# Optimization experiments

Measured on AMD Instinct MI355X. Metric: run time of the kernel, lower is better.

The kernel has to match this reference:

```python
import jax, jax.numpy as jnp
import numpy as np

K = 3.0  # power parameter k from __init__

def _weight1_sq(d2, r):
    # weight1 on squared distances: (1 - (d/r)^2)^k where d < r, else 0
    r2 = r * r
    flag = d2 < r2
    base = jnp.where(flag, 1.0 - d2 / r2, 0.0)  # >= 0 where flag
    return jnp.where(flag, base ** K, 0.0)

def _weight2(d, r):
    half = r * 0.5
    in1 = d < half
    in2 = (d >= half) & (d < r)
    d_safe = jnp.where(in2, d, half)  # keep base in [0,1] outside the branch
    t = (2.0 * d_safe - r) / r
    w2 = (1.0 - t * t) ** K
    return jnp.where(in1, 1.0, jnp.where(in2, w2, 0.0))

def _normalize(w):
    return w / jnp.sum(w, axis=0, keepdims=True)


def setup_inputs() -> dict:
    key = jax.random.key(0)
    n, p = 4096, 64
    x = jax.random.normal(key, (n, p), dtype=jnp.float32)
    return {
        "x": x,
        "r0": jnp.float32(12.0),
        "r1": jnp.float32(11.0),
        "r2": jnp.float32(12.0),
    }


def reference(x, r0, r1, r2):
    y = x  # y = x.clone(); purely functional here
    sq = jnp.sum(x * x, axis=1)
    # squared pairwise distances (cdist^2), clamped for numerical safety
    d2 = jnp.maximum(sq[:, None] + sq[None, :] - 2.0 * (x @ x.T), 0.0)  # (n, n)
    max_dist = jnp.sqrt(jnp.max(d2))
    # parameter reassignment r := min(r, max_dist)
    r0 = jnp.minimum(r0, max_dist)
    r1 = jnp.minimum(r1, max_dist)
    r2 = jnp.minimum(r2, max_dist)
    # row selection inds: dist[i,i] = 0 <= r0 always, so all rows are kept (identity)
    alpha = _normalize(_weight1_sq(d2, r0))  # (n, n)
    mu = alpha.T @ x  # (n, p)
    mu = jnp.where(jnp.isnan(mu), y, mu)
    U = y - mu  # (n, p), contraction directions
    # projection[i,j] = c_ij * U_j with c_ij = (x_i - y_j) . U_j
    c = x @ U.T - jnp.sum(y * U, axis=1)[None, :]  # (n, n)
    du = c * c * jnp.sum(U * U, axis=1)[None, :]   # ||projection||^2, (n, n)
    du = jnp.maximum(du, 1e-6)
    dv = jnp.sqrt(jnp.maximum(d2 - du, 1e-6))
    du = jnp.sqrt(du)
    beta = _normalize(_weight2(dv, r1) * _weight2(du, r2))  # (n, n)
    e_Z = beta.T @ x  # (n, p)
    return jnp.where(jnp.isnan(e_Z), y, e_Z)
```

## Files before the change

kernel.cpp:

```cpp
#include <hip/hip_runtime.h>
#include <stdint.h>

typedef unsigned short u16;
typedef short bf16x8 __attribute__((ext_vector_type(8)));
typedef unsigned short u16x4 __attribute__((ext_vector_type(4)));
typedef float f32x4 __attribute__((ext_vector_type(4)));

#define NROW 4096
#define LDW 72
#define SLICE 262144
#define NSPLIT 8

__device__ __forceinline__ u16 f2bf(float f) {
  uint32_t u = __float_as_uint(f);
  u = (u + 0x7fffu + ((u >> 16) & 1u)) >> 16;
  return (u16)u;
}

__device__ __forceinline__ u16 f2bf_t(float f) {
  return (u16)(__float_as_uint(f) >> 16);
}

__device__ __forceinline__ f32x4 mfma16(bf16x8 a, bf16x8 b, f32x4 c) {
  return __builtin_amdgcn_mfma_f32_16x16x32_bf16(a, b, c, 0, 0, 0);
}

__device__ __forceinline__ bf16x8 ld8(const u16* p) {
  return *reinterpret_cast<const bf16x8*>(p);
}

__device__ __forceinline__ float fast_sqrt(float x) {
  return __builtin_amdgcn_sqrtf(x);
}

__device__ __forceinline__ float slots_max(const float* __restrict__ maxslots, int lane) {
  float md = maxslots[lane * 16];
#pragma unroll
  for (int o = 1; o < 64; o <<= 1) md = fmaxf(md, __shfl_xor(md, o));
  return md;
}

__global__ __launch_bounds__(256) void prep_kernel(const float* __restrict__ x,
                                                   u16* __restrict__ xb, u16* __restrict__ xT,
                                                   float* __restrict__ sq,
                                                   float* __restrict__ maxslots) {
  __shared__ u16 lt[64 * 68];
  __shared__ float pmax[4];
  const int tid = threadIdx.x, w = tid >> 6, lane = tid & 63;
  const int r0 = blockIdx.x * 64;
  const int rl = tid >> 2;
  const int g = tid & 3;
  const int row = r0 + rl;

  const float* xr = x + row * 64 + g * 16;
  const float* x0 = x + g * 16;
  float s = 0.f, s2 = 0.f;
  u16 bb[16];
#pragma unroll
  for (int k = 0; k < 4; ++k) {
    float4 v = *reinterpret_cast<const float4*>(xr + k * 4);
    float4 z = *reinterpret_cast<const float4*>(x0 + k * 4);
    s += v.x * v.x + v.y * v.y + v.z * v.z + v.w * v.w;
    float dx = v.x - z.x, dy = v.y - z.y, dz = v.z - z.z, dw = v.w - z.w;
    s2 += dx * dx + dy * dy + dz * dz + dw * dw;
    bb[k * 4 + 0] = f2bf(v.x);
    bb[k * 4 + 1] = f2bf(v.y);
    bb[k * 4 + 2] = f2bf(v.z);
    bb[k * 4 + 3] = f2bf(v.w);
  }
#pragma unroll
  for (int k = 0; k < 4; ++k) {
    u16x4 p;
    p[0] = bb[k * 4]; p[1] = bb[k * 4 + 1]; p[2] = bb[k * 4 + 2]; p[3] = bb[k * 4 + 3];
    *reinterpret_cast<u16x4*>(&xb[row * 64 + g * 16 + k * 4]) = p;
  }
#pragma unroll
  for (int k = 0; k < 16; ++k) lt[(g * 16 + k) * 68 + rl] = bb[k];
  s += __shfl_xor(s, 1);
  s += __shfl_xor(s, 2);
  s2 += __shfl_xor(s2, 1);
  s2 += __shfl_xor(s2, 2);
  if (g == 0) sq[row] = s;
  float wm = s2;
#pragma unroll
  for (int o = 4; o < 64; o <<= 1) wm = fmaxf(wm, __shfl_xor(wm, o));
  if (lane == 0) pmax[w] = wm;
  __syncthreads();
#pragma unroll
  for (int cc = 0; cc < 16; ++cc) {
    int c = w * 16 + cc;
    xT[c * NROW + r0 + lane] = lt[c * 68 + lane];
  }
  if (tid == 0)
    maxslots[blockIdx.x * 16] = fmaxf(fmaxf(pmax[0], pmax[1]), fmaxf(pmax[2], pmax[3]));
}

__global__ __launch_bounds__(256) void pass1_max(const u16* __restrict__ xb,
                                                 const float* __restrict__ sq,
                                                 float* __restrict__ maxslots,
                                                 const float* __restrict__ r0in,
                                                 const float* __restrict__ r1in,
                                                 const float* __restrict__ r2in) {
  __shared__ float red[4];
  int w = threadIdx.x >> 6, lane = threadIdx.x & 63;
  {
    float lb = slots_max(maxslots, lane);
    float rmax = fmaxf(fmaxf(r0in[0], r1in[0]), r2in[0]);
    if (lb >= rmax * rmax) return;
  }
  int l16 = lane & 15, quad = lane >> 4;
  int ti = blockIdx.x;
  int i0 = ti * 64 + w * 16;
  bf16x8 a0 = ld8(xb + (i0 + l16) * 64 + quad * 8);
  bf16x8 a1 = ld8(xb + (i0 + l16) * 64 + 32 + quad * 8);
  float sqi[4];
#pragma unroll
  for (int r = 0; r < 4; ++r) sqi[r] = sq[i0 + quad * 4 + r];
  float m = 0.f;
  const int jbase = blockIdx.y * 256;
#pragma unroll
  for (int jb = 0; jb < 4; ++jb) {
    int j0 = jbase + jb * 64;
#pragma unroll
    for (int jt = 0; jt < 4; ++jt) {
      int jr = j0 + jt * 16 + l16;
      bf16x8 b0 = ld8(xb + jr * 64 + quad * 8);
      bf16x8 b1 = ld8(xb + jr * 64 + 32 + quad * 8);
      f32x4 g = {0.f, 0.f, 0.f, 0.f};
      g = mfma16(a0, b0, g);
      g = mfma16(a1, b1, g);
      float sj = sq[jr];
#pragma unroll
      for (int r = 0; r < 4; ++r) m = fmaxf(m, fmaf(-2.f, g[r], sqi[r] + sj));
    }
  }
  m = fmaxf(m, 0.f);
#pragma unroll
  for (int o = 1; o < 64; o <<= 1) m = fmaxf(m, __shfl_xor(m, o));
  if (lane == 0) red[w] = m;
  __syncthreads();
  if (threadIdx.x == 0) {
    m = fmaxf(fmaxf(red[0], red[1]), fmaxf(red[2], red[3]));
    atomicMax((int*)&maxslots[ti * 16], __float_as_int(m));
  }
}

__global__ __launch_bounds__(256, 2) void pass2_kernel(
    const u16* __restrict__ xb, const u16* __restrict__ xT, const float* __restrict__ sq,
    const float* __restrict__ maxslots, const float* __restrict__ r0in,
    float* __restrict__ mu_part, float* __restrict__ s_part) {
  __shared__ u16 ldsw[2][64 * LDW];
  __shared__ u16 xjt[64 * LDW];
  __shared__ float sred[4][64];
  const int tid = threadIdx.x, w = tid >> 6, lane = tid & 63;
  const int l16 = lane & 15, quad = lane >> 4;
  const int j0 = blockIdx.x * 64;
  const int ibase = blockIdx.y * 512;

#pragma unroll
  for (int k = 0; k < 2; ++k) {
    int ch = tid + k * 256;
    int row = ch >> 3, c8 = ch & 7;
    *reinterpret_cast<bf16x8*>(&xjt[row * LDW + c8 * 8]) = ld8(xb + (j0 + row) * 64 + c8 * 8);
  }

  const float md = slots_max(maxslots, lane);
  const float r0c = fminf(r0in[0], fast_sqrt(md));
  const float invr0sq = 1.f / (r0c * r0c);

  float sqj[4];
#pragma unroll
  for (int jt = 0; jt < 4; ++jt) sqj[jt] = sq[j0 + jt * 16 + l16];

  f32x4 zero4 = {0.f, 0.f, 0.f, 0.f};
  f32x4 acc[4];
#pragma unroll
  for (int pt = 0; pt < 4; ++pt) acc[pt] = zero4;
  float sa[4] = {0.f, 0.f, 0.f, 0.f};

  auto do_weights = [&](bf16x8 A0, bf16x8 A1, float4 QI, u16* wbuf) {
#pragma unroll
    for (int jp = 0; jp < 2; ++jp) {
      const int jt0 = jp * 2, jt1 = jp * 2 + 1;
      f32x4 g0 = zero4, g1 = zero4;
      bf16x8 x00 = ld8(&xjt[(jt0 * 16 + l16) * LDW + quad * 8]);
      bf16x8 x10 = ld8(&xjt[(jt1 * 16 + l16) * LDW + quad * 8]);
      bf16x8 x01 = ld8(&xjt[(jt0 * 16 + l16) * LDW + 32 + quad * 8]);
      bf16x8 x11 = ld8(&xjt[(jt1 * 16 + l16) * LDW + 32 + quad * 8]);
      g0 = mfma16(A0, x00, g0);
      g1 = mfma16(A0, x10, g1);
      g0 = mfma16(A1, x01, g0);
      g1 = mfma16(A1, x11, g1);
      u16x4 pk0, pk1;
#pragma unroll
      for (int r = 0; r < 4; ++r) {
        float d2a = fmaxf(fmaf(-2.f, g0[r], QI[r] + sqj[jt0]), 0.f);
        float ba = fmaxf(fmaf(-d2a, invr0sq, 1.f), 0.f);
        float wa = ba * ba * ba;
        sa[jt0] += wa;
        pk0[r] = f2bf_t(wa);
        float d2b = fmaxf(fmaf(-2.f, g1[r], QI[r] + sqj[jt1]), 0.f);
        float bb = fmaxf(fmaf(-d2b, invr0sq, 1.f), 0.f);
        float wb = bb * bb * bb;
        sa[jt1] += wb;
        pk1[r] = f2bf_t(wb);
      }
      *reinterpret_cast<u16x4*>(&wbuf[(jt0 * 16 + l16) * LDW + w * 16 + quad * 4]) = pk0;
      *reinterpret_cast<u16x4*>(&wbuf[(jt1 * 16 + l16) * LDW + w * 16 + quad * 4]) = pk1;
    }
  };

  const int ir0 = ibase + w * 16;
  bf16x8 p0 = ld8(xb + (ir0 + l16) * 64 + quad * 8);
  bf16x8 p1 = ld8(xb + (ir0 + l16) * 64 + 32 + quad * 8);
  float4 q0 = *reinterpret_cast<const float4*>(&sq[ir0 + quad * 4]);
  __syncthreads();
  do_weights(p0, p1, q0, &ldsw[0][0]);
  bf16x8 a0 = ld8(xb + (ir0 + 64 + l16) * 64 + quad * 8);
  bf16x8 a1 = ld8(xb + (ir0 + 64 + l16) * 64 + 32 + quad * 8);
  float4 qi = *reinterpret_cast<const float4*>(&sq[ir0 + 64 + quad * 4]);
  __syncthreads();

#pragma unroll
  for (int s = 0; s < 8; ++s) {
    u16* rbuf = &ldsw[s & 1][0];
    const int ib = ibase + s * 64;
    bf16x8 aw0 = ld8(&rbuf[(w * 16 + l16) * LDW + quad * 8]);
    bf16x8 aw1 = ld8(&rbuf[(w * 16 + l16) * LDW + 32 + quad * 8]);
    const u16* xp0 = xT + (0 * 16 + l16) * NROW + ib + quad * 8;
    const u16* xp1 = xT + (1 * 16 + l16) * NROW + ib + quad * 8;
    const u16* xp2 = xT + (2 * 16 + l16) * NROW + ib + quad * 8;
    const u16* xp3 = xT + (3 * 16 + l16) * NROW + ib + quad * 8;
    bf16x8 t00 = ld8(xp0), t01 = ld8(xp0 + 32);
    bf16x8 t10 = ld8(xp1), t11 = ld8(xp1 + 32);
    bf16x8 t20 = ld8(xp2), t21 = ld8(xp2 + 32);
    bf16x8 t30 = ld8(xp3), t31 = ld8(xp3 + 32);
    if (s < 7) {
      do_weights(a0, a1, qi, &ldsw[(s + 1) & 1][0]);
      if (s < 6) {
        const int irn = ibase + (s + 2) * 64 + w * 16;
        a0 = ld8(xb + (irn + l16) * 64 + quad * 8);
        a1 = ld8(xb + (irn + l16) * 64 + 32 + quad * 8);
        qi = *reinterpret_cast<const float4*>(&sq[irn + quad * 4]);
      }
    }
    acc[0] = mfma16(aw0, t00, acc[0]);
    acc[0] = mfma16(aw1, t01, acc[0]);
    acc[1] = mfma16(aw0, t10, acc[1]);
    acc[1] = mfma16(aw1, t11, acc[1]);
    acc[2] = mfma16(aw0, t20, acc[2]);
    acc[2] = mfma16(aw1, t21, acc[2]);
    acc[3] = mfma16(aw0, t30, acc[3]);
    acc[3] = mfma16(aw1, t31, acc[3]);
    __syncthreads();
  }
  float* mp = mu_part + (size_t)blockIdx.y * SLICE;
#pragma unroll
  for (int pt = 0; pt < 4; ++pt)
#pragma unroll
    for (int r = 0; r < 4; ++r)
      mp[(j0 + w * 16 + quad * 4 + r) * 64 + pt * 16 + l16] = acc[pt][r];
#pragma unroll
  for (int jt = 0; jt < 4; ++jt) {
    float v = sa[jt];
    v += __shfl_xor(v, 16);
    v += __shfl_xor(v, 32);
    if (lane < 16) sred[w][jt * 16 + lane] = v;
  }
  __syncthreads();
  if (tid < 64)
    s_part[blockIdx.y * NROW + j0 + tid] =
        sred[0][tid] + sred[1][tid] + sred[2][tid] + sred[3][tid];
}

__global__ __launch_bounds__(256, 2) void pass3_kernel(
    const u16* __restrict__ xb, const u16* __restrict__ xT, const float* __restrict__ sq,
    const float* __restrict__ mu_part, const float* __restrict__ s_part_a,
    const float* __restrict__ maxslots, const float* __restrict__ r1in,
    const float* __restrict__ r2in, const float* __restrict__ x,
    float* __restrict__ ez_part, float* __restrict__ s_part) {
  __shared__ u16 ldsw[2][64 * LDW];
  __shared__ u16 xjt[64 * LDW];
  __shared__ u16 ujt[64 * LDW];
  __shared__ float sred[4][64];
  __shared__ float tj_s[64], u2_s[64];
  const int tid = threadIdx.x, w = tid >> 6, lane = tid & 63;
  const int l16 = lane & 15, quad = lane >> 4;
  const int j0 = blockIdx.x * 64;
  const int ibase = blockIdx.y * 512;

#pragma unroll
  for (int k = 0; k < 2; ++k) {
    int ch = tid + k * 256;
    int row = ch >> 3, c8 = ch & 7;
    *reinterpret_cast<bf16x8*>(&xjt[row * LDW + c8 * 8]) = ld8(xb + (j0 + row) * 64 + c8 * 8);
  }

  {
    const int rl16 = tid >> 4;
    const int c4 = tid & 15;
#pragma unroll
    for (int sw = 0; sw < 4; ++sw) {
      const int lrow = sw * 16 + rl16;
      const int row = j0 + lrow;
      float4 num = {0.f, 0.f, 0.f, 0.f};
      float den = 0.f;
#pragma unroll
      for (int y = 0; y < NSPLIT; ++y) {
        float4 v =
            *reinterpret_cast<const float4*>(&mu_part[(size_t)y * SLICE + row * 64 + c4 * 4]);
        num.x += v.x; num.y += v.y; num.z += v.z; num.w += v.w;
        den += s_part_a[y * NROW + row];
      }
      float4 xv = *reinterpret_cast<const float4*>(&x[row * 64 + c4 * 4]);
      float inv = 1.f / den;
      float m0 = num.x * inv, m1 = num.y * inv, m2 = num.z * inv, m3 = num.w * inv;
      if (m0 != m0) m0 = xv.x;
      if (m1 != m1) m1 = xv.y;
      if (m2 != m2) m2 = xv.z;
      if (m3 != m3) m3 = xv.w;
      float U0 = xv.x - m0, U1 = xv.y - m1, U2 = xv.z - m2, U3 = xv.w - m3;
      u16x4 pb;
      pb[0] = f2bf(U0); pb[1] = f2bf(U1); pb[2] = f2bf(U2); pb[3] = f2bf(U3);
      *reinterpret_cast<u16x4*>(&ujt[lrow * LDW + c4 * 4]) = pb;
      float aa = U0 * U0 + U1 * U1 + U2 * U2 + U3 * U3;
      float bb = xv.x * U0 + xv.y * U1 + xv.z * U2 + xv.w * U3;
#pragma unroll
      for (int o = 1; o < 16; o <<= 1) {
        aa += __shfl_xor(aa, o);
        bb += __shfl_xor(bb, o);
      }
      if (c4 == 0) {
        u2_s[lrow] = aa;
        tj_s[lrow] = bb;
      }
    }
  }

  const float md = slots_max(maxslots, lane);
  const float mdist = fast_sqrt(md);
  const float r1c = fminf(r1in[0], mdist);
  const float r2c = fminf(r2in[0], mdist);
  const float i1x2 = 2.f / r1c;
  const float i2x2 = 2.f / r2c;

  f32x4 zero4 = {0.f, 0.f, 0.f, 0.f};
  f32x4 acc[4];
#pragma unroll
  for (int pt = 0; pt < 4; ++pt) acc[pt] = zero4;
  float sb[4] = {0.f, 0.f, 0.f, 0.f};

  const int ir0 = ibase + w * 16;
  bf16x8 p0 = ld8(xb + (ir0 + l16) * 64 + quad * 8);
  bf16x8 p1 = ld8(xb + (ir0 + l16) * 64 + 32 + quad * 8);
  float4 q0 = *reinterpret_cast<const float4*>(&sq[ir0 + quad * 4]);
  __syncthreads();

  float sqj[4], tj[4], u2j[4];
#pragma unroll
  for (int jt = 0; jt < 4; ++jt) {
    sqj[jt] = sq[j0 + jt * 16 + l16];
    tj[jt] = tj_s[jt * 16 + l16];
    u2j[jt] = u2_s[jt * 16 + l16];
  }

  auto do_weights = [&](bf16x8 A0, bf16x8 A1, float4 QI, u16* wbuf) {
#pragma unroll
    for (int jt = 0; jt < 4; ++jt) {
      f32x4 gxx = zero4, gxu = zero4;
      bf16x8 xf0 = ld8(&xjt[(jt * 16 + l16) * LDW + quad * 8]);
      bf16x8 uf0 = ld8(&ujt[(jt * 16 + l16) * LDW + quad * 8]);
      bf16x8 xf1 = ld8(&xjt[(jt * 16 + l16) * LDW + 32 + quad * 8]);
      bf16x8 uf1 = ld8(&ujt[(jt * 16 + l16) * LDW + 32 + quad * 8]);
      gxx = mfma16(A0, xf0, gxx);
      gxu = mfma16(A0, uf0, gxu);
      gxx = mfma16(A1, xf1, gxx);
      gxu = mfma16(A1, uf1, gxu);
      const float tjv = tj[jt], u2jv = u2j[jt], sjv = sqj[jt];
      u16x4 pk;
#pragma unroll
      for (int r = 0; r < 4; ++r) {
        float d2 = fmaxf(fmaf(-2.f, gxx[r], QI[r] + sjv), 0.f);
        float c = gxu[r] - tjv;
        float du2 = fmaxf(c * c * u2jv, 1e-6f);
        float dv2 = fmaxf(d2 - du2, 1e-6f);
        float du = fast_sqrt(du2);
        float dv = fast_sqrt(dv2);
        float q1 = fminf(fmaxf(fmaf(dv, i1x2, -1.f), 0.f), 1.f);
        float b1 = fmaf(-q1, q1, 1.f);
        float w1 = b1 * b1 * b1;
        float q2 = fminf(fmaxf(fmaf(du, i2x2, -1.f), 0.f), 1.f);
        float b2 = fmaf(-q2, q2, 1.f);
        float w2 = b2 * b2 * b2;
        float wv = w1 * w2;
        sb[jt] += wv;
        pk[r] = f2bf_t(wv);
      }
      *reinterpret_cast<u16x4*>(&wbuf[(jt * 16 + l16) * LDW + w * 16 + quad * 4]) = pk;
    }
  };

  do_weights(p0, p1, q0, &ldsw[0][0]);
  bf16x8 a0 = ld8(xb + (ir0 + 64 + l16) * 64 + quad * 8);
  bf16x8 a1 = ld8(xb + (ir0 + 64 + l16) * 64 + 32 + quad * 8);
  float4 qi = *reinterpret_cast<const float4*>(&sq[ir0 + 64 + quad * 4]);
  __syncthreads();

#pragma unroll
  for (int s = 0; s < 8; ++s) {
    u16* rbuf = &ldsw[s & 1][0];
    const int ib = ibase + s * 64;
    bf16x8 aw0 = ld8(&rbuf[(w * 16 + l16) * LDW + quad * 8]);
    bf16x8 aw1 = ld8(&rbuf[(w * 16 + l16) * LDW + 32 + quad * 8]);
    const u16* xp0 = xT + (0 * 16 + l16) * NROW + ib + quad * 8;
    const u16* xp1 = xT + (1 * 16 + l16) * NROW + ib + quad * 8;
    const u16* xp2 = xT + (2 * 16 + l16) * NROW + ib + quad * 8;
    const u16* xp3 = xT + (3 * 16 + l16) * NROW + ib + quad * 8;
    bf16x8 t00 = ld8(xp0), t01 = ld8(xp0 + 32);
    bf16x8 t10 = ld8(xp1), t11 = ld8(xp1 + 32);
    bf16x8 t20 = ld8(xp2), t21 = ld8(xp2 + 32);
    bf16x8 t30 = ld8(xp3), t31 = ld8(xp3 + 32);
    if (s < 7) {
      do_weights(a0, a1, qi, &ldsw[(s + 1) & 1][0]);
      if (s < 6) {
        const int irn = ibase + (s + 2) * 64 + w * 16;
        a0 = ld8(xb + (irn + l16) * 64 + quad * 8);
        a1 = ld8(xb + (irn + l16) * 64 + 32 + quad * 8);
        qi = *reinterpret_cast<const float4*>(&sq[irn + quad * 4]);
      }
    }
    acc[0] = mfma16(aw0, t00, acc[0]);
    acc[0] = mfma16(aw1, t01, acc[0]);
    acc[1] = mfma16(aw0, t10, acc[1]);
    acc[1] = mfma16(aw1, t11, acc[1]);
    acc[2] = mfma16(aw0, t20, acc[2]);
    acc[2] = mfma16(aw1, t21, acc[2]);
    acc[3] = mfma16(aw0, t30, acc[3]);
    acc[3] = mfma16(aw1, t31, acc[3]);
    __syncthreads();
  }
  float* ep = ez_part + (size_t)blockIdx.y * SLICE;
#pragma unroll
  for (int pt = 0; pt < 4; ++pt)
#pragma unroll
    for (int r = 0; r < 4; ++r)
      ep[(j0 + w * 16 + quad * 4 + r) * 64 + pt * 16 + l16] = acc[pt][r];
#pragma unroll
  for (int jt = 0; jt < 4; ++jt) {
    float v = sb[jt];
    v += __shfl_xor(v, 16);
    v += __shfl_xor(v, 32);
    if (lane < 16) sred[w][jt * 16 + lane] = v;
  }
  __syncthreads();
  if (tid < 64)
    s_part[blockIdx.y * NROW + j0 + tid] =
        sred[0][tid] + sred[1][tid] + sred[2][tid] + sred[3][tid];
}

__global__ __launch_bounds__(256) void finish_kernel(const float* __restrict__ x,
                                                     const float* __restrict__ ez_part,
                                                     const float* __restrict__ s_part,
                                                     float* __restrict__ out) {
  const int tid = threadIdx.x;
  const int row = blockIdx.x * 16 + (tid >> 4);
  const int c4 = tid & 15;
  float4 num = {0.f, 0.f, 0.f, 0.f};
  float den = 0.f;
#pragma unroll
  for (int y = 0; y < NSPLIT; ++y) {
    float4 v = *reinterpret_cast<const float4*>(&ez_part[(size_t)y * SLICE + row * 64 + c4 * 4]);
    num.x += v.x; num.y += v.y; num.z += v.z; num.w += v.w;
    den += s_part[y * NROW + row];
  }
  float4 xv = *reinterpret_cast<const float4*>(&x[row * 64 + c4 * 4]);
  float inv = 1.f / den;
  float4 o;
  o.x = num.x * inv; o.y = num.y * inv; o.z = num.z * inv; o.w = num.w * inv;
  if (o.x != o.x) o.x = xv.x;
  if (o.y != o.y) o.y = xv.y;
  if (o.z != o.z) o.z = xv.z;
  if (o.w != o.w) o.w = xv.w;
  *reinterpret_cast<float4*>(&out[row * 64 + c4 * 4]) = o;
}

extern "C" void kernel_launch(void* const* d_in, const int* in_sizes, int n_in,
                              void* d_out, int out_size, void* d_ws, size_t ws_size,
                              hipStream_t stream) {
  (void)in_sizes; (void)n_in; (void)out_size;
  const float* x = (const float*)d_in[0];
  const float* r0 = (const float*)d_in[1];
  const float* r1 = (const float*)d_in[2];
  const float* r2 = (const float*)d_in[3];
  float* out = (float*)d_out;
  char* ws = (char*)d_ws;

  u16* xb = (u16*)(ws);
  u16* xT = (u16*)(ws + (512 << 10));
  float* sq = (float*)(ws + (1536 << 10));
  float* maxslots = (float*)(ws + (1584 << 10));
  float* s_part_a = (float*)(ws + (1588 << 10));
  float* s_part_b = (float*)(ws + (1844 << 10));
  float* part_mu = (float*)(ws + (2100 << 10));
  float* part_ez = (float*)(ws + ((2100 << 10) + ((size_t)8 << 20)));
  size_t need = ((size_t)2100 << 10) + ((size_t)16 << 20);
  if (ws_size < need) return;

  prep_kernel<<<64, 256, 0, stream>>>(x, xb, xT, sq, maxslots);
  pass1_max<<<dim3(64, 16), 256, 0, stream>>>(xb, sq, maxslots, r0, r1, r2);
  pass2_kernel<<<dim3(64, NSPLIT), 256, 0, stream>>>(xb, xT, sq, maxslots, r0, part_mu,
                                                     s_part_a);
  pass3_kernel<<<dim3(64, NSPLIT), 256, 0, stream>>>(xb, xT, sq, part_mu, s_part_a, maxslots,
                                                     r1, r2, x, part_ez, s_part_b);
  finish_kernel<<<256, 256, 0, stream>>>(x, part_ez, s_part_b, out);
}
```

Measured before the change: 121.6 us.

## Feed weight fragments straight from registers into MFMA, dropping LDS weight staging

In pass2 and pass3, the computed weight tile no longer goes through a double-buffered LDS transpose. Each wave feeds its own 16-row weight fragment directly as the A operand of 16x16x16 bf16 MFMAs, accumulating a full 64x64 partial per wave. A cross-wave LDS reduction runs once at the end. This removes the per-step __syncthreads and LDS write/read of the weights, but it quadruples accumulator registers (64 floats per lane), uses a smaller-K MFMA, and gives up the software pipelining between the weight stage and the accumulate stage.

Measured after the change: 114.4 us. 1.06x faster.

```diff
diff --git a/kernel.cpp b/kernel.cpp
--- a/kernel.cpp
+++ b/kernel.cpp
@@ -3,11 +3,13 @@
 
 typedef unsigned short u16;
 typedef short bf16x8 __attribute__((ext_vector_type(8)));
+typedef short s16x4 __attribute__((ext_vector_type(4)));
 typedef unsigned short u16x4 __attribute__((ext_vector_type(4)));
 typedef float f32x4 __attribute__((ext_vector_type(4)));
 
 #define NROW 4096
 #define LDW 72
+#define RDW 68
 #define SLICE 262144
 #define NSPLIT 8
 
@@ -23,6 +25,10 @@
 
 __device__ __forceinline__ f32x4 mfma16(bf16x8 a, bf16x8 b, f32x4 c) {
   return __builtin_amdgcn_mfma_f32_16x16x32_bf16(a, b, c, 0, 0, 0);
+}
+
+__device__ __forceinline__ f32x4 mfma16k(s16x4 a, s16x4 b, f32x4 c) {
+  return __builtin_amdgcn_mfma_f32_16x16x16bf16_1k(a, b, c, 0, 0, 0);
 }
 
 __device__ __forceinline__ bf16x8 ld8(const u16* p) {
@@ -149,8 +155,8 @@
     const u16* __restrict__ xb, const u16* __restrict__ xT, const float* __restrict__ sq,
     const float* __restrict__ maxslots, const float* __restrict__ r0in,
     float* __restrict__ mu_part, float* __restrict__ s_part) {
-  __shared__ u16 ldsw[2][64 * LDW];
   __shared__ u16 xjt[64 * LDW];
+  __shared__ float redbuf[4][32 * RDW];
   __shared__ float sred[4][64];
   const int tid = threadIdx.x, w = tid >> 6, lane = tid & 63;
   const int l16 = lane & 15, quad = lane >> 4;
@@ -173,93 +179,83 @@
   for (int jt = 0; jt < 4; ++jt) sqj[jt] = sq[j0 + jt * 16 + l16];
 
   f32x4 zero4 = {0.f, 0.f, 0.f, 0.f};
-  f32x4 acc[4];
-#pragma unroll
-  for (int pt = 0; pt < 4; ++pt) acc[pt] = zero4;
+  f32x4 acc[4][4];
+#pragma unroll
+  for (int jt = 0; jt < 4; ++jt)
+#pragma unroll
+    for (int pt = 0; pt < 4; ++pt) acc[jt][pt] = zero4;
   float sa[4] = {0.f, 0.f, 0.f, 0.f};
 
-  auto do_weights = [&](bf16x8 A0, bf16x8 A1, float4 QI, u16* wbuf) {
-#pragma unroll
-    for (int jp = 0; jp < 2; ++jp) {
-      const int jt0 = jp * 2, jt1 = jp * 2 + 1;
-      f32x4 g0 = zero4, g1 = zero4;
-      bf16x8 x00 = ld8(&xjt[(jt0 * 16 + l16) * LDW + quad * 8]);
-      bf16x8 x10 = ld8(&xjt[(jt1 * 16 + l16) * LDW + quad * 8]);
-      bf16x8 x01 = ld8(&xjt[(jt0 * 16 + l16) * LDW + 32 + quad * 8]);
-      bf16x8 x11 = ld8(&xjt[(jt1 * 16 + l16) * LDW + 32 + quad * 8]);
-      g0 = mfma16(A0, x00, g0);
-      g1 = mfma16(A0, x10, g1);
-      g0 = mfma16(A1, x01, g0);
-      g1 = mfma16(A1, x11, g1);
-      u16x4 pk0, pk1;
+  const int iw0 = ibase + w * 16;
+  bf16x8 a0 = ld8(xb + (iw0 + l16) * 64 + quad * 8);
+  bf16x8 a1 = ld8(xb + (iw0 + l16) * 64 + 32 + quad * 8);
+  float4 qi = *reinterpret_cast<const float4*>(&sq[iw0 + quad * 4]);
+  __syncthreads();
+
+#pragma unroll
+  for (int s = 0; s < 8; ++s) {
+    const int ib_w = ibase + s * 64 + w * 16;
+    bf16x8 na0, na1;
+    float4 nqi;
+    if (s < 7) {
+      const int irn = ibase + (s + 1) * 64 + w * 16;
+      na0 = ld8(xb + (irn + l16) * 64 + quad * 8);
+      na1 = ld8(xb + (irn + l16) * 64 + 32 + quad * 8);
+      nqi = *reinterpret_cast<const float4*>(&sq[irn + quad * 4]);
+    }
+    s16x4 bfr[4];
+#pragma unroll
+    for (int pt = 0; pt < 4; ++pt)
+      bfr[pt] =
+          *reinterpret_cast<const s16x4*>(xT + (pt * 16 + l16) * NROW + ib_w + quad * 4);
+#pragma unroll
+    for (int jt = 0; jt < 4; ++jt) {
+      bf16x8 xj0 = ld8(&xjt[(jt * 16 + l16) * LDW + quad * 8]);
+      bf16x8 xj1 = ld8(&xjt[(jt * 16 + l16) * LDW + 32 + quad * 8]);
+      f32x4 g = zero4;
+      g = mfma16(a0, xj0, g);
+      g = mfma16(a1, xj1, g);
+      s16x4 wf;
 #pragma unroll
       for (int r = 0; r < 4; ++r) {
-        float d2a = fmaxf(fmaf(-2.f, g0[r], QI[r] + sqj[jt0]), 0.f);
-        float ba = fmaxf(fmaf(-d2a, invr0sq, 1.f), 0.f);
-        float wa = ba * ba * ba;
-        sa[jt0] += wa;
-        pk0[r] = f2bf_t(wa);
-        float d2b = fmaxf(fmaf(-2.f, g1[r], QI[r] + sqj[jt1]), 0.f);
-        float bb = fmaxf(fmaf(-d2b, invr0sq, 1.f), 0.f);
-        float wb = bb * bb * bb;
-        sa[jt1] += wb;
-        pk1[r] = f2bf_t(wb);
+        float d2 = fmaxf(fmaf(-2.f, g[r], qi[r] + sqj[jt]), 0.f);
+        float ba = fmaxf(fmaf(-d2, invr0sq, 1.f), 0.f);
+        float wv = ba * ba * ba;
+        sa[jt] += wv;
+        wf[r] = (short)f2bf_t(wv);
       }
-      *reinterpret_cast<u16x4*>(&wbuf[(jt0 * 16 + l16) * LDW + w * 16 + quad * 4]) = pk0;
-      *reinterpret_cast<u16x4*>(&wbuf[(jt1 * 16 + l16) * LDW + w * 16 + quad * 4]) = pk1;
-    }
-  };
-
-  const int ir0 = ibase + w * 16;
-  bf16x8 p0 = ld8(xb + (ir0 + l16) * 64 + quad * 8);
-  bf16x8 p1 = ld8(xb + (ir0 + l16) * 64 + 32 + quad * 8);
-  float4 q0 = *reinterpret_cast<const float4*>(&sq[ir0 + quad * 4]);
-  __syncthreads();
-  do_weights(p0, p1, q0, &ldsw[0][0]);
-  bf16x8 a0 = ld8(xb + (ir0 + 64 + l16) * 64 + quad * 8);
-  bf16x8 a1 = ld8(xb + (ir0 + 64 + l16) * 64 + 32 + quad * 8);
-  float4 qi = *reinterpret_cast<const float4*>(&sq[ir0 + 64 + quad * 4]);
-  __syncthreads();
-
-#pragma unroll
-  for (int s = 0; s < 8; ++s) {
-    u16* rbuf = &ldsw[s & 1][0];
-    const int ib = ibase + s * 64;
-    bf16x8 aw0 = ld8(&rbuf[(w * 16 + l16) * LDW + quad * 8]);
-    bf16x8 aw1 = ld8(&rbuf[(w * 16 + l16) * LDW + 32 + quad * 8]);
-    const u16* xp0 = xT + (0 * 16 + l16) * NROW + ib + quad * 8;
-    const u16* xp1 = xT + (1 * 16 + l16) * NROW + ib + quad * 8;
-    const u16* xp2 = xT + (2 * 16 + l16) * NROW + ib + quad * 8;
-    const u16* xp3 = xT + (3 * 16 + l16) * NROW + ib + quad * 8;
-    bf16x8 t00 = ld8(xp0), t01 = ld8(xp0 + 32);
-    bf16x8 t10 = ld8(xp1), t11 = ld8(xp1 + 32);
-    bf16x8 t20 = ld8(xp2), t21 = ld8(xp2 + 32);
-    bf16x8 t30 = ld8(xp3), t31 = ld8(xp3 + 32);
+#pragma unroll
+      for (int pt = 0; pt < 4; ++pt) acc[jt][pt] = mfma16k(wf, bfr[pt], acc[jt][pt]);
+    }
     if (s < 7) {
-      do_weights(a0, a1, qi, &ldsw[(s + 1) & 1][0]);
-      if (s < 6) {
-        const int irn = ibase + (s + 2) * 64 + w * 16;
-        a0 = ld8(xb + (irn + l16) * 64 + quad * 8);
-        a1 = ld8(xb + (irn + l16) * 64 + 32 + quad * 8);
-        qi = *reinterpret_cast<const float4*>(&sq[irn + quad * 4]);
-      }
-    }
-    acc[0] = mfma16(aw0, t00, acc[0]);
-    acc[0] = mfma16(aw1, t01, acc[0]);
-    acc[1] = mfma16(aw0, t10, acc[1]);
-    acc[1] = mfma16(aw1, t11, acc[1]);
-    acc[2] = mfma16(aw0, t20, acc[2]);
-    acc[2] = mfma16(aw1, t21, acc[2]);
-    acc[3] = mfma16(aw0, t30, acc[3]);
-    acc[3] = mfma16(aw1, t31, acc[3]);
+      a0 = na0;
+      a1 = na1;
+      qi = nqi;
+    }
+  }
+
+  float* mp = mu_part + (size_t)blockIdx.y * SLICE;
+#pragma unroll
+  for (int rd = 0; rd < 2; ++rd) {
     __syncthreads();
-  }
-  float* mp = mu_part + (size_t)blockIdx.y * SLICE;
-#pragma unroll
-  for (int pt = 0; pt < 4; ++pt)
-#pragma unroll
-    for (int r = 0; r < 4; ++r)
-      mp[(j0 + w * 16 + quad * 4 + r) * 64 + pt * 16 + l16] = acc[pt][r];
+#pragma unroll
+    for (int jh = 0; jh < 2; ++jh) {
+      const int jt = rd * 2 + jh;
+#pragma unroll
+      for (int pt = 0; pt < 4; ++pt)
+#pragma unroll
+        for (int r = 0; r < 4; ++r)
+          redbuf[w][(jh * 16 + quad * 4 + r) * RDW + pt * 16 + l16] = acc[jt][pt][r];
+    }
+    __syncthreads();
+#pragma unroll
+    for (int jj = 0; jj < 8; ++jj) {
+      const int jrel = w * 8 + jj;
+      float v = redbuf[0][jrel * RDW + lane] + redbuf[1][jrel * RDW + lane] +
+                redbuf[2][jrel * RDW + lane] + redbuf[3][jrel * RDW + lane];
+      mp[(j0 + rd * 32 + jrel) * 64 + lane] = v;
+    }
+  }
 #pragma unroll
   for (int jt = 0; jt < 4; ++jt) {
     float v = sa[jt];
@@ -279,9 +275,9 @@
     const float* __restrict__ maxslots, const float* __restrict__ r1in,
     const float* __restrict__ r2in, const float* __restrict__ x,
     float* __restrict__ ez_part, float* __restrict__ s_part) {
-  __shared__ u16 ldsw[2][64 * LDW];
   __shared__ u16 xjt[64 * LDW];
   __shared__ u16 ujt[64 * LDW];
+  __shared__ float redbuf[4][32 * RDW];
   __shared__ float sred[4][64];
   __shared__ float tj_s[64], u2_s[64];
   const int tid = threadIdx.x, w = tid >> 6, lane = tid & 63;
@@ -345,15 +341,17 @@
   const float i2x2 = 2.f / r2c;
 
   f32x4 zero4 = {0.f, 0.f, 0.f, 0.f};
-  f32x4 acc[4];
-#pragma unroll
-  for (int pt = 0; pt < 4; ++pt) acc[pt] = zero4;
+  f32x4 acc[4][4];
+#pragma unroll
+  for (int jt = 0; jt < 4; ++jt)
+#pragma unroll
+    for (int pt = 0; pt < 4; ++pt) acc[jt][pt] = zero4;
   float sb[4] = {0.f, 0.f, 0.f, 0.f};
 
-  const int ir0 = ibase + w * 16;
-  bf16x8 p0 = ld8(xb + (ir0 + l16) * 64 + quad * 8);
-  bf16x8 p1 = ld8(xb + (ir0 + l16) * 64 + 32 + quad * 8);
-  float4 q0 = *reinterpret_cast<const float4*>(&sq[ir0 + quad * 4]);
+  const int iw0 = ibase + w * 16;
+  bf16x8 a0 = ld8(xb + (iw0 + l16) * 64 + quad * 8);
+  bf16x8 a1 = ld8(xb + (iw0 + l16) * 64 + 32 + quad * 8);
+  float4 qi = *reinterpret_cast<const float4*>(&sq[iw0 + quad * 4]);
   __syncthreads();
 
   float sqj[4], tj[4], u2j[4];
@@ -364,23 +362,38 @@
     u2j[jt] = u2_s[jt * 16 + l16];
   }
 
-  auto do_weights = [&](bf16x8 A0, bf16x8 A1, float4 QI, u16* wbuf) {
+#pragma unroll
+  for (int s = 0; s < 8; ++s) {
+    const int ib_w = ibase + s * 64 + w * 16;
+    bf16x8 na0, na1;
+    float4 nqi;
+    if (s < 7) {
+      const int irn = ibase + (s + 1) * 64 + w * 16;
+      na0 = ld8(xb + (irn + l16) * 64 + quad * 8);
+      na1 = ld8(xb + (irn + l16) * 64 + 32 + quad * 8);
+      nqi = *reinterpret_cast<const float4*>(&sq[irn + quad * 4]);
+    }
+    s16x4 bfr[4];
+#pragma unroll
+    for (int pt = 0; pt < 4; ++pt)
+      bfr[pt] =
+          *reinterpret_cast<const s16x4*>(xT + (pt * 16 + l16) * NROW + ib_w + quad * 4);
 #pragma unroll
     for (int jt = 0; jt < 4; ++jt) {
-      f32x4 gxx = zero4, gxu = zero4;
       bf16x8 xf0 = ld8(&xjt[(jt * 16 + l16) * LDW + quad * 8]);
       bf16x8 uf0 = ld8(&ujt[(jt * 16 + l16) * LDW + quad * 8]);
       bf16x8 xf1 = ld8(&xjt[(jt * 16 + l16) * LDW + 32 + quad * 8]);
       bf16x8 uf1 = ld8(&ujt[(jt * 16 + l16) * LDW + 32 + quad * 8]);
-      gxx = mfma16(A0, xf0, gxx);
-      gxu = mfma16(A0, uf0, gxu);
-      gxx = mfma16(A1, xf1, gxx);
-      gxu = mfma16(A1, uf1, gxu);
+      f32x4 gxx = zero4, gxu = zero4;
+      gxx = mfma16(a0, xf0, gxx);
+      gxu = mfma16(a0, uf0, gxu);
+      gxx = mfma16(a1, xf1, gxx);
+      gxu = mfma16(a1, uf1, gxu);
       const float tjv = tj[jt], u2jv = u2j[jt], sjv = sqj[jt];
-      u16x4 pk;
+      s16x4 wf;
 #pragma unroll
       for (int r = 0; r < 4; ++r) {
-        float d2 = fmaxf(fmaf(-2.f, gxx[r], QI[r] + sjv), 0.f);
+        float d2 = fmaxf(fmaf(-2.f, gxx[r], qi[r] + sjv), 0.f);
         float c = gxu[r] - tjv;
         float du2 = fmaxf(c * c * u2jv, 1e-6f);
         float dv2 = fmaxf(d2 - du2, 1e-6f);
@@ -394,57 +407,40 @@
         float w2 = b2 * b2 * b2;
         float wv = w1 * w2;
         sb[jt] += wv;
-        pk[r] = f2bf_t(wv);
+        wf[r] = (short)f2bf_t(wv);
       }
-      *reinterpret_cast<u16x4*>(&wbuf[(jt * 16 + l16) * LDW + w * 16 + quad * 4]) = pk;
-    }
-  };
-
-  do_weights(p0, p1, q0, &ldsw[0][0]);
-  bf16x8 a0 = ld8(xb + (ir0 + 64 + l16) * 64 + quad * 8);
-  bf16x8 a1 = ld8(xb + (ir0 + 64 + l16) * 64 + 32 + quad * 8);
-  float4 qi = *reinterpret_cast<const float4*>(&sq[ir0 + 64 + quad * 4]);
-  __syncthreads();
-
-#pragma unroll
-  for (int s = 0; s < 8; ++s) {
-    u16* rbuf = &ldsw[s & 1][0];
-    const int ib = ibase + s * 64;
-    bf16x8 aw0 = ld8(&rbuf[(w * 16 + l16) * LDW + quad * 8]);
-    bf16x8 aw1 = ld8(&rbuf[(w * 16 + l16) * LDW + 32 + quad * 8]);
-    const u16* xp0 = xT + (0 * 16 + l16) * NROW + ib + quad * 8;
-    const u16* xp1 = xT + (1 * 16 + l16) * NROW + ib + quad * 8;
-    const u16* xp2 = xT + (2 * 16 + l16) * NROW + ib + quad * 8;
-    const u16* xp3 = xT + (3 * 16 + l16) * NROW + ib + quad * 8;
-    bf16x8 t00 = ld8(xp0), t01 = ld8(xp0 + 32);
-    bf16x8 t10 = ld8(xp1), t11 = ld8(xp1 + 32);
-    bf16x8 t20 = ld8(xp2), t21 = ld8(xp2 + 32);
-    bf16x8 t30 = ld8(xp3), t31 = ld8(xp3 + 32);
+#pragma unroll
+      for (int pt = 0; pt < 4; ++pt) acc[jt][pt] = mfma16k(wf, bfr[pt], acc[jt][pt]);
+    }
     if (s < 7) {
-      do_weights(a0, a1, qi, &ldsw[(s + 1) & 1][0]);
-      if (s < 6) {
-        const int irn = ibase + (s + 2) * 64 + w * 16;
-        a0 = ld8(xb + (irn + l16) * 64 + quad * 8);
-        a1 = ld8(xb + (irn + l16) * 64 + 32 + quad * 8);
-        qi = *reinterpret_cast<const float4*>(&sq[irn + quad * 4]);
-      }
-    }
-    acc[0] = mfma16(aw0, t00, acc[0]);
-    acc[0] = mfma16(aw1, t01, acc[0]);
-    acc[1] = mfma16(aw0, t10, acc[1]);
-    acc[1] = mfma16(aw1, t11, acc[1]);
-    acc[2] = mfma16(aw0, t20, acc[2]);
-    acc[2] = mfma16(aw1, t21, acc[2]);
-    acc[3] = mfma16(aw0, t30, acc[3]);
-    acc[3] = mfma16(aw1, t31, acc[3]);
+      a0 = na0;
+      a1 = na1;
+      qi = nqi;
+    }
+  }
+
+  float* ep = ez_part + (size_t)blockIdx.y * SLICE;
+#pragma unroll
+  for (int rd = 0; rd < 2; ++rd) {
     __syncthreads();
-  }
-  float* ep = ez_part + (size_t)blockIdx.y * SLICE;
-#pragma unroll
-  for (int pt = 0; pt < 4; ++pt)
-#pragma unroll
-    for (int r = 0; r < 4; ++r)
-      ep[(j0 + w * 16 + quad * 4 + r) * 64 + pt * 16 + l16] = acc[pt][r];
+#pragma unroll
+    for (int jh = 0; jh < 2; ++jh) {
+      const int jt = rd * 2 + jh;
+#pragma unroll
+      for (int pt = 0; pt < 4; ++pt)
+#pragma unroll
+        for (int r = 0; r < 4; ++r)
+          redbuf[w][(jh * 16 + quad * 4 + r) * RDW + pt * 16 + l16] = acc[jt][pt][r];
+    }
+    __syncthreads();
+#pragma unroll
+    for (int jj = 0; jj < 8; ++jj) {
+      const int jrel = w * 8 + jj;
+      float v = redbuf[0][jrel * RDW + lane] + redbuf[1][jrel * RDW + lane] +
+                redbuf[2][jrel * RDW + lane] + redbuf[3][jrel * RDW + lane];
+      ep[(j0 + rd * 32 + jrel) * 64 + lane] = v;
+    }
+  }
 #pragma unroll
   for (int jt = 0; jt < 4; ++jt) {
     float v = sb[jt];
```
